# Optimization experiments

Hardware: AMD Instinct MI355X
Metric: run time of the kernel (lower is better)

Reference implementation:

```python
import jax, jax.numpy as jnp
import numpy as np
from jax import lax

G = 8        # group_num
BS = 32      # blocksize
SC = 13      # sample_channel = round(32*32*0.1/8)


def conv2d(x, w, b=None, stride=1, pad=0):
    y = lax.conv_general_dilated(x, w, (stride, stride), [(pad, pad), (pad, pad)],
                                 dimension_numbers=("NCHW", "OIHW", "NCHW"))
    if b is not None:
        y = y + b[None, :, None, None]
    return y


def prelu(x, a):
    return jnp.where(x >= 0, x, a * x)


def depth_to_space(x, bs):
    # matches Reshape_Concat_Adap: channel index = c_out*bs*bs + i*bs + j
    b, c, h, w = x.shape
    co = c // (bs * bs)
    x = x.reshape(b, co, bs, bs, h, w)
    x = x.transpose(0, 1, 4, 2, 5, 3)  # b, co, h, bs, w, bs
    return x.reshape(b, co, h * bs, w * bs)


def setup_inputs() -> dict:
    key = jax.random.key(0)
    ks = jax.random.split(key, 16)
    s = 0.05
    inp = {
        "x": jax.random.normal(ks[0], (8, 1, 256, 256), jnp.float32),
        "sample_w": jax.random.normal(ks[1], (G, SC, 1, BS, BS), jnp.float32) * 0.02,
        "up_w": jax.random.normal(ks[2], (G, BS * BS, SC, 1, 1), jnp.float32) * s,
        "up_b": jnp.zeros((G, BS * BS), jnp.float32),
        "conv1_w": jax.random.normal(ks[3], (G, 64, 1, 3, 3), jnp.float32) * s,
        "conv1_b": jnp.zeros((G, 64), jnp.float32),
        "conv1_a": jnp.full((G,), 0.25, jnp.float32),
        "fus_w": jax.random.normal(ks[4], (G - 1, 64, 128, 3, 3), jnp.float32) * s,
        "fus_b": jnp.zeros((G - 1, 64), jnp.float32),
        "fus_a": jnp.full((G - 1,), 0.25, jnp.float32),
        "t2_w": jax.random.normal(ks[5], (G, 64, 64, 3, 3), jnp.float32) * s,
        "t2_b": jnp.zeros((G, 64), jnp.float32),
        "t2_a": jnp.full((G,), 0.25, jnp.float32),
        "t3_w": jax.random.normal(ks[6], (G, 64, 64, 3, 3), jnp.float32) * s,
        "t3_b": jnp.zeros((G, 64), jnp.float32),
        "t3_a": jnp.full((G,), 0.25, jnp.float32),
        "t4_w": jax.random.normal(ks[7], (G, 64, 64, 3, 3), jnp.float32) * s,
        "t4_b": jnp.zeros((G, 64), jnp.float32),
        "t4_a": jnp.full((G,), 0.25, jnp.float32),
        "t5_w": jax.random.normal(ks[8], (G, 1, 64, 3, 3), jnp.float32) * s,
        "t5_b": jnp.zeros((G, 1), jnp.float32),
    }
    return inp


def reference(x, sample_w, up_w, up_b, conv1_w, conv1_b, conv1_a,
              fus_w, fus_b, fus_a, t2_w, t2_b, t2_a, t3_w, t3_b, t3_a,
              t4_w, t4_b, t4_a, t5_w, t5_b):
    def head(g):
        y = conv2d(x, sample_w[g], stride=BS)              # [B,SC,H/32,W/32]
        y = conv2d(y, up_w[g], up_b[g])                    # [B,1024,H/32,W/32]
        y = depth_to_space(y, BS)                          # [B,1,H,W]
        return prelu(conv2d(y, conv1_w[g], conv1_b[g], pad=1), conv1_a[g])

    def tail(h, g):
        h = prelu(conv2d(h, t2_w[g], t2_b[g], pad=1), t2_a[g])
        h = prelu(conv2d(h, t3_w[g], t3_b[g], pad=1), t3_a[g])
        h = prelu(conv2d(h, t4_w[g], t4_b[g], pad=1), t4_a[g])
        return conv2d(h, t5_w[g], t5_b[g], pad=1)          # [B,1,H,W]

    heads = [head(g) for g in range(G)]
    cur = heads[0]
    outs = [tail(cur, 0)]
    for m in range(G - 1):
        cat = jnp.concatenate([cur, heads[m + 1]], axis=1)  # [B,128,H,W]
        cur = prelu(conv2d(cat, fus_w[m], fus_b[m], pad=1), fus_a[m])
        outs.append(tail(cur, m + 1))
    return jnp.stack(outs, axis=0)  # [G,B,1,H,W]
```

## Files before the change

kernel.cpp:

```cpp
#include <hip/hip_runtime.h>
#include <stdint.h>

typedef __attribute__((ext_vector_type(8))) short short8;
typedef __attribute__((ext_vector_type(16))) float floatx16;

#define PLANE 16777216

__device__ __forceinline__ float b2f(short s) {
  union { uint32_t u; float f; } v; v.u = ((uint32_t)(uint16_t)s) << 16; return v.f;
}
__device__ __forceinline__ short f2b(float f) {
  union { float f; uint32_t u; } v; v.f = f;
  uint32_t r = (v.u + 0x7FFFu + ((v.u >> 16) & 1u)) >> 16;
  return (short)r;
}

__device__ __forceinline__ uint32_t ldsAddr(int r, int xp, int c) {
  uint32_t byte = ((uint32_t)(r * 258 + xp) << 6) + ((uint32_t)c << 1);
  byte ^= ((uint32_t)(xp & 7)) << 4;
  return byte;
}

template<int NCHUNK>
__global__ __launch_bounds__(512)
void k_conv(const short* __restrict__ in1, const short* __restrict__ in2,
            const short* __restrict__ wp, const float* __restrict__ bias,
            const float* __restrict__ alpha, short* __restrict__ out)
{
  __shared__ __align__(16) uint8_t smem[4 * 258 * 64];
  const int y0 = blockIdx.x * 2, b = blockIdx.y;
  const int tid = threadIdx.x;
  const int l = tid & 63;
  const int w = tid >> 6;
  const int pxhalf = w & 1;
  const int nblk = (w >> 1) & 1;
  const int yrow = w >> 2;
  const int lm = l & 31;
  const int lh = l >> 5;

  floatx16 acc[4];
  #pragma unroll
  for (int mf = 0; mf < 4; ++mf)
    #pragma unroll
    for (int r = 0; r < 16; ++r) acc[mf][r] = 0.f;

  const int xbase = pxhalf * 128 + lm;

  for (int q = 0; q < NCHUNK; ++q) {
    const short* __restrict__ src = ((q < 2) ? in1 : in2) + (size_t)(q & 1) * PLANE;

    __syncthreads();
    for (int widx = tid; widx < 4 * 258 * 4; widx += 512) {
      int r = widx / (258 * 4);
      int rem = widx - r * (258 * 4);
      int xp = rem >> 2;
      int co = (rem & 3) << 3;
      int xx = xp - 1;
      int yy = y0 + r - 1;
      short8 v = {0, 0, 0, 0, 0, 0, 0, 0};
      if ((unsigned)xx < 256u && (unsigned)yy < 256u)
        v = *(const short8*)(src + ((b * 256 + yy) * 256 + xx) * 32 + co);
      *(short8*)(smem + ldsAddr(r, xp, co)) = v;
    }
    __syncthreads();

    #pragma unroll
    for (int ky = 0; ky < 3; ++ky)
    #pragma unroll
    for (int kx = 0; kx < 3; ++kx)
    #pragma unroll
    for (int s = 0; s < 2; ++s) {
      const int ks = (q * 9 + ky * 3 + kx) * 2 + s;
      const short8 bw = *(const short8*)(wp + ((ks * 2 + nblk) * 64 + l) * 8);
      const int cl = s * 16 + lh * 8;
      #pragma unroll
      for (int mf = 0; mf < 4; ++mf) {
        const int xp = xbase + mf * 32 + kx;
        const short8 av = *(const short8*)(smem + ldsAddr(yrow + ky, xp, cl));
        acc[mf] = __builtin_amdgcn_mfma_f32_32x32x16_bf16(av, bw, acc[mf], 0, 0, 0);
      }
    }
  }

  const float alp = alpha[0];
  const int cout = nblk * 32 + lm;
  const float bs = bias[cout];
  const int y = y0 + yrow;
  short* __restrict__ op = out + (size_t)nblk * PLANE + lm;
  #pragma unroll
  for (int mf = 0; mf < 4; ++mf) {
    #pragma unroll
    for (int r = 0; r < 16; ++r) {
      int px = pxhalf * 128 + mf * 32 + (r & 3) + ((r >> 2) << 3) + (lh << 2);
      float v = acc[mf][r] + bs;
      v = v >= 0.f ? v : alp * v;
      op[((b * 256 + y) * 256 + px) * 32] = f2b(v);
      op += 0;
    }
  }
}

__global__ __launch_bounds__(256)
void k_pack(const float* __restrict__ w2, const float* __restrict__ w3,
            const float* __restrict__ w4, const float* __restrict__ wf,
            short* __restrict__ wp234, short* __restrict__ wpfus)
{
  int idx = blockIdx.x * 256 + threadIdx.x;
  if (idx < 24 * 36864) {
    int conv = idx / 36864;
    int r = idx - conv * 36864;
    int which = conv >> 3, g = conv & 7;
    const float* W = (which == 0 ? w2 : which == 1 ? w3 : w4) + g * 36864;
    int ks = r >> 10;
    int nblk = (r >> 9) & 1;
    int lane = (r >> 3) & 63;
    int e = r & 7;
    int q = ks / 18, tt = ks % 18;
    int t = tt >> 1, s = tt & 1;
    int cin = q * 32 + s * 16 + ((lane >> 5) << 3) + e;
    int cout = nblk * 32 + (lane & 31);
    int ky = t / 3, kx = t % 3;
    wp234[idx] = f2b(W[((cout * 64 + cin) * 3 + ky) * 3 + kx]);
  } else {
    int idx2 = idx - 24 * 36864;
    if (idx2 >= 7 * 73728) return;
    int conv = idx2 / 73728;
    int r = idx2 - conv * 73728;
    const float* W = wf + conv * 73728;
    int ks = r >> 10;
    int nblk = (r >> 9) & 1;
    int lane = (r >> 3) & 63;
    int e = r & 7;
    int q = ks / 18, tt = ks % 18;
    int t = tt >> 1, s = tt & 1;
    int cin = q * 32 + s * 16 + ((lane >> 5) << 3) + e;
    int cout = nblk * 32 + (lane & 31);
    int ky = t / 3, kx = t % 3;
    wpfus[idx2] = f2b(W[((cout * 128 + cin) * 3 + ky) * 3 + kx]);
  }
}

__global__ __launch_bounds__(256)
void k_sample(const float* __restrict__ x, const float* __restrict__ sw,
              float* __restrict__ s_all)
{
  int idx = blockIdx.x * 256 + threadIdx.x;
  int gx = idx & 7, gy = (idx >> 3) & 7;
  int t = idx >> 6;
  int c = t % 13; t /= 13;
  int b = t & 7, g = t >> 3;
  const float* xb = x + b * 65536 + (gy * 32) * 256 + gx * 32;
  const float* wp = sw + (g * 13 + c) * 1024;
  float acc = 0.f;
  for (int i = 0; i < 32; ++i) {
    #pragma unroll
    for (int j = 0; j < 32; ++j) acc += xb[i * 256 + j] * wp[i * 32 + j];
  }
  s_all[idx] = acc;
}

__global__ __launch_bounds__(256)
void k_upz(const float* __restrict__ s_all, const float* __restrict__ upw,
           const float* __restrict__ upb, float* __restrict__ z_all)
{
  int idx = blockIdx.x * 256 + threadIdx.x;
  int x = idx & 255, y = (idx >> 8) & 255;
  int b = (idx >> 16) & 7, g = idx >> 19;
  int pos = (y & 31) * 32 + (x & 31);
  int gy = y >> 5, gx = x >> 5;
  const float* sp = s_all + ((g * 8 + b) * 13) * 64 + gy * 8 + gx;
  const float* wp = upw + (g * 1024 + pos) * 13;
  float a = upb[g * 1024 + pos];
  #pragma unroll
  for (int c = 0; c < 13; ++c) a += wp[c] * sp[c * 64];
  z_all[idx] = a;
}

__global__ __launch_bounds__(256)
void k_conv1(const float* __restrict__ z, const float* __restrict__ w,
             const float* __restrict__ bias, const float* __restrict__ alpha,
             short* __restrict__ out)
{
  int pid = blockIdx.x * 256 + threadIdx.x;
  int x = pid & 255, y = (pid >> 8) & 255, b = pid >> 16;
  float zv[9];
  #pragma unroll
  for (int t = 0; t < 9; ++t) {
    int dy = t / 3, dx = t % 3;
    int yy = y + dy - 1, xx = x + dx - 1;
    zv[t] = ((unsigned)yy < 256u && (unsigned)xx < 256u)
              ? z[b * 65536 + yy * 256 + xx] : 0.f;
  }
  float alp = alpha[0];
  #pragma unroll
  for (int c0 = 0; c0 < 64; c0 += 8) {
    short8 pack;
    #pragma unroll
    for (int e = 0; e < 8; ++e) {
      int c = c0 + e;
      float a = bias[c];
      #pragma unroll
      for (int t = 0; t < 9; ++t) a += w[c * 9 + t] * zv[t];
      a = a >= 0.f ? a : alp * a;
      pack[e] = f2b(a);
    }
    *(short8*)(out + (size_t)(c0 >> 5) * PLANE + pid * 32 + (c0 & 31)) = pack;
  }
}

__global__ __launch_bounds__(256)
void k_t5(const short* __restrict__ in, const float* __restrict__ w,
          const float* __restrict__ bias, float* __restrict__ out)
{
  int pid = blockIdx.x * 256 + threadIdx.x;
  int x = pid & 255, y = (pid >> 8) & 255, b = pid >> 16;
  float acc = bias[0];
  for (int dy = 0; dy < 3; ++dy) {
    int yy = y + dy - 1;
    if ((unsigned)yy >= 256u) continue;
    for (int dx = 0; dx < 3; ++dx) {
      int xx = x + dx - 1;
      if ((unsigned)xx >= 256u) continue;
      const int pix = (b * 256 + yy) * 256 + xx;
      #pragma unroll
      for (int c0 = 0; c0 < 64; c0 += 8) {
        short8 v = *(const short8*)(in + (size_t)(c0 >> 5) * PLANE + pix * 32 + (c0 & 31));
        #pragma unroll
        for (int e = 0; e < 8; ++e)
          acc += w[(c0 + e) * 9 + dy * 3 + dx] * b2f(v[e]);
      }
    }
  }
  out[pid] = acc;
}

extern "C" void kernel_launch(void* const* d_in, const int* in_sizes, int n_in,
                              void* d_out, int out_size, void* d_ws, size_t ws_size,
                              hipStream_t stream) {
  const float* X   = (const float*)d_in[0];
  const float* SW  = (const float*)d_in[1];
  const float* UPW = (const float*)d_in[2];
  const float* UPB = (const float*)d_in[3];
  const float* C1W = (const float*)d_in[4];
  const float* C1B = (const float*)d_in[5];
  const float* C1A = (const float*)d_in[6];
  const float* FW  = (const float*)d_in[7];
  const float* FB  = (const float*)d_in[8];
  const float* FA  = (const float*)d_in[9];
  const float* W2  = (const float*)d_in[10];
  const float* B2  = (const float*)d_in[11];
  const float* A2  = (const float*)d_in[12];
  const float* W3  = (const float*)d_in[13];
  const float* B3  = (const float*)d_in[14];
  const float* A3  = (const float*)d_in[15];
  const float* W4  = (const float*)d_in[16];
  const float* B4  = (const float*)d_in[17];
  const float* A4  = (const float*)d_in[18];
  const float* W5  = (const float*)d_in[19];
  const float* B5  = (const float*)d_in[20];
  float* OUT = (float*)d_out;
  (void)in_sizes; (void)n_in; (void)out_size; (void)ws_size;

  uint8_t* base = (uint8_t*)d_ws;
  size_t off = 0;
  auto alloc = [&](size_t bytes) -> uint8_t* {
    uint8_t* r = base + off;
    off += (bytes + 255) & ~(size_t)255;
    return r;
  };
  const size_t ACT_ELEMS = 2ull * PLANE;
  short* act[3];
  for (int i = 0; i < 3; ++i) act[i] = (short*)alloc(ACT_ELEMS * 2);
  float* z_all = (float*)alloc(4194304ull * 4);
  float* s_all = (float*)alloc(53248ull * 4);
  short* wp234 = (short*)alloc(884736ull * 2);
  short* wpfus = (short*)alloc(516096ull * 2);

  k_pack<<<dim3(5472), dim3(256), 0, stream>>>(W2, W3, W4, FW, wp234, wpfus);
  k_sample<<<dim3(208), dim3(256), 0, stream>>>(X, SW, s_all);
  k_upz<<<dim3(16384), dim3(256), 0, stream>>>(s_all, UPW, UPB, z_all);

  int cur = 0, A = 1, B = 2;
  k_conv1<<<dim3(2048), dim3(256), 0, stream>>>(z_all, C1W, C1B, C1A, act[cur]);

  for (int m = 0; m < 8; ++m) {
    const short* wp_t2 = wp234 + (0 * 8 + m) * 36864;
    const short* wp_t3 = wp234 + (1 * 8 + m) * 36864;
    const short* wp_t4 = wp234 + (2 * 8 + m) * 36864;

    k_conv<2><<<dim3(128, 8), dim3(512), 0, stream>>>(
        act[cur], act[cur], wp_t2, B2 + m * 64, A2 + m, act[A]);
    k_conv<2><<<dim3(128, 8), dim3(512), 0, stream>>>(
        act[A], act[A], wp_t3, B3 + m * 64, A3 + m, act[B]);
    k_conv<2><<<dim3(128, 8), dim3(512), 0, stream>>>(
        act[B], act[B], wp_t4, B4 + m * 64, A4 + m, act[A]);
    k_t5<<<dim3(2048), dim3(256), 0, stream>>>(
        act[A], W5 + m * 576, B5 + m, OUT + (size_t)m * 524288);

    if (m < 7) {
      k_conv1<<<dim3(2048), dim3(256), 0, stream>>>(
          z_all + (size_t)(m + 1) * 524288, C1W + (m + 1) * 576,
          C1B + (m + 1) * 64, C1A + (m + 1), act[B]);
      k_conv<4><<<dim3(128, 8), dim3(512), 0, stream>>>(
          act[cur], act[B], wpfus + m * 73728, FB + m * 64, FA + m, act[A]);
      int tmp = cur; cur = A; A = tmp;
    }
  }
}
```

Before: 3.303 ms.

## Prefetch next input chunk into registers and remap warps to share A fragments

Software-pipelines the conv halo load: the next channel chunk is issued into registers before the MFMA loop on the current chunk and committed to LDS afterwards, overlapping global loads with compute. Warps are remapped so each computes both 32-channel output blocks for 64 pixels, reusing each A fragment across two MFMAs, which halves LDS A reads per MFMA at the cost of two weight loads. Halo columns are zeroed once instead of on every chunk. Launch bounds now request 4 waves per SIMD. The register staging (8 short8 per thread) raises register pressure, which could cause spills under the tighter bound.

```diff
diff --git a/kernel.cpp b/kernel.cpp
--- a/kernel.cpp
+++ b/kernel.cpp
@@ -22,7 +22,7 @@
 }
 
 template<int NCHUNK>
-__global__ __launch_bounds__(512)
+__global__ __launch_bounds__(512, 4)
 void k_conv(const short* __restrict__ in1, const short* __restrict__ in2,
             const short* __restrict__ wp, const float* __restrict__ bias,
             const float* __restrict__ alpha, short* __restrict__ out)
@@ -32,9 +32,8 @@
   const int tid = threadIdx.x;
   const int l = tid & 63;
   const int w = tid >> 6;
-  const int pxhalf = w & 1;
-  const int nblk = (w >> 1) & 1;
-  const int yrow = w >> 2;
+  const int yrow = w & 1;
+  const int pxq = w >> 1;
   const int lm = l & 31;
   const int lh = l >> 5;
 
@@ -44,25 +43,53 @@
     #pragma unroll
     for (int r = 0; r < 16; ++r) acc[mf][r] = 0.f;
 
-  const int xbase = pxhalf * 128 + lm;
-
-  for (int q = 0; q < NCHUNK; ++q) {
+  const int xbase = pxq * 64 + lm;
+
+  short8 stg[8];
+  const int s_r  = tid >> 10;
+  (void)s_r;
+
+  auto issue = [&](int q) {
     const short* __restrict__ src = ((q < 2) ? in1 : in2) + (size_t)(q & 1) * PLANE;
-
-    __syncthreads();
-    for (int widx = tid; widx < 4 * 258 * 4; widx += 512) {
-      int r = widx / (258 * 4);
-      int rem = widx - r * (258 * 4);
-      int xp = rem >> 2;
-      int co = (rem & 3) << 3;
-      int xx = xp - 1;
+    #pragma unroll
+    for (int i = 0; i < 8; ++i) {
+      int widx = tid + i * 512;
+      int r = widx >> 10;
+      int xp = ((widx >> 2) & 255) + 1;
+      int co = (widx & 3) << 3;
       int yy = y0 + r - 1;
       short8 v = {0, 0, 0, 0, 0, 0, 0, 0};
-      if ((unsigned)xx < 256u && (unsigned)yy < 256u)
-        v = *(const short8*)(src + ((b * 256 + yy) * 256 + xx) * 32 + co);
-      *(short8*)(smem + ldsAddr(r, xp, co)) = v;
-    }
-    __syncthreads();
+      if ((unsigned)yy < 256u)
+        v = *(const short8*)(src + ((b * 256 + yy) * 256 + (xp - 1)) * 32 + co);
+      stg[i] = v;
+    }
+  };
+  auto commit = [&]() {
+    #pragma unroll
+    for (int i = 0; i < 8; ++i) {
+      int widx = tid + i * 512;
+      int r = widx >> 10;
+      int xp = ((widx >> 2) & 255) + 1;
+      int co = (widx & 3) << 3;
+      *(short8*)(smem + ldsAddr(r, xp, co)) = stg[i];
+    }
+  };
+
+  if (tid < 32) {
+    short8 z = {0, 0, 0, 0, 0, 0, 0, 0};
+    int r = tid >> 3;
+    int xp = (tid & 4) ? 257 : 0;
+    int co = (tid & 3) << 3;
+    *(short8*)(smem + ldsAddr(r, xp, co)) = z;
+  }
+
+  issue(0);
+  commit();
+  __syncthreads();
+
+  #pragma unroll
+  for (int q = 0; q < NCHUNK; ++q) {
+    if (q + 1 < NCHUNK) issue(q + 1);
 
     #pragma unroll
     for (int ky = 0; ky < 3; ++ky)
@@ -71,31 +98,40 @@
     #pragma unroll
     for (int s = 0; s < 2; ++s) {
       const int ks = (q * 9 + ky * 3 + kx) * 2 + s;
-      const short8 bw = *(const short8*)(wp + ((ks * 2 + nblk) * 64 + l) * 8);
+      const short8 bw0 = *(const short8*)(wp + ((ks * 2 + 0) * 64 + l) * 8);
+      const short8 bw1 = *(const short8*)(wp + ((ks * 2 + 1) * 64 + l) * 8);
       const int cl = s * 16 + lh * 8;
       #pragma unroll
-      for (int mf = 0; mf < 4; ++mf) {
+      for (int mf = 0; mf < 2; ++mf) {
         const int xp = xbase + mf * 32 + kx;
         const short8 av = *(const short8*)(smem + ldsAddr(yrow + ky, xp, cl));
-        acc[mf] = __builtin_amdgcn_mfma_f32_32x32x16_bf16(av, bw, acc[mf], 0, 0, 0);
+        acc[mf * 2 + 0] = __builtin_amdgcn_mfma_f32_32x32x16_bf16(av, bw0, acc[mf * 2 + 0], 0, 0, 0);
+        acc[mf * 2 + 1] = __builtin_amdgcn_mfma_f32_32x32x16_bf16(av, bw1, acc[mf * 2 + 1], 0, 0, 0);
       }
     }
+
+    if (q + 1 < NCHUNK) {
+      __syncthreads();
+      commit();
+      __syncthreads();
+    }
   }
 
   const float alp = alpha[0];
-  const int cout = nblk * 32 + lm;
-  const float bs = bias[cout];
   const int y = y0 + yrow;
-  short* __restrict__ op = out + (size_t)nblk * PLANE + lm;
-  #pragma unroll
-  for (int mf = 0; mf < 4; ++mf) {
-    #pragma unroll
-    for (int r = 0; r < 16; ++r) {
-      int px = pxhalf * 128 + mf * 32 + (r & 3) + ((r >> 2) << 3) + (lh << 2);
-      float v = acc[mf][r] + bs;
-      v = v >= 0.f ? v : alp * v;
-      op[((b * 256 + y) * 256 + px) * 32] = f2b(v);
-      op += 0;
+  #pragma unroll
+  for (int nb = 0; nb < 2; ++nb) {
+    const float bs = bias[nb * 32 + lm];
+    short* __restrict__ op = out + (size_t)nb * PLANE + lm;
+    #pragma unroll
+    for (int mf = 0; mf < 2; ++mf) {
+      #pragma unroll
+      for (int r = 0; r < 16; ++r) {
+        int px = pxq * 64 + mf * 32 + (r & 3) + ((r >> 2) << 3) + (lh << 2);
+        float v = acc[mf * 2 + nb][r] + bs;
+        v = v >= 0.f ? v : alp * v;
+        op[((b * 256 + y) * 256 + px) * 32] = f2b(v);
+      }
     }
   }
 }
```

Measured after the change: 4.033 ms. +22.1%, slower.
